# Optimization experiments

Hardware: AMD Instinct MI355X
Metric: run time of the kernel (lower is better)

The kernel has to match this reference:

```python
import jax, jax.numpy as jnp
import numpy as np

N_NODES = 100000
N_EDGES = 1600000
N_GRAPHS = 64
D_IN = 64
D_HID = 64
D_OUT = 64


def gcn_conv(x, W, b, src, dst, n):
    """PyG-style GCNConv: x' = D^-1/2 (A+I) D^-1/2 (x W) + b."""
    xw = x @ W  # [N, d_out]
    loops = jnp.arange(n, dtype=src.dtype)
    s = jnp.concatenate([src, loops])  # add self-loops
    d = jnp.concatenate([dst, loops])
    deg = jax.ops.segment_sum(jnp.ones_like(d, dtype=xw.dtype), d, num_segments=n)
    dinv = jax.lax.rsqrt(jnp.maximum(deg, 1.0))
    coef = dinv[s] * dinv[d]  # [E+N]
    msg = xw[s] * coef[:, None]  # gather + scale, [E+N, d_out]
    out = jax.ops.segment_sum(msg, d, num_segments=n)  # scatter-add
    return out + b


def global_mean_pool(h, batch, num_graphs):
    sums = jax.ops.segment_sum(h, batch, num_segments=num_graphs)
    cnt = jax.ops.segment_sum(jnp.ones((h.shape[0],), h.dtype), batch, num_segments=num_graphs)
    return sums / jnp.maximum(cnt, 1.0)[:, None]


def setup_inputs() -> dict:
    key = jax.random.key(0)
    ks = jax.random.split(key, 8)
    x = jax.random.normal(ks[0], (N_NODES, D_IN), dtype=jnp.float32)
    edge_index = jax.random.randint(ks[1], (2, N_EDGES), 0, N_NODES, dtype=jnp.int64 if jax.config.jax_enable_x64 else jnp.int32)
    batch = jnp.sort(jax.random.randint(ks[2], (N_NODES,), 0, N_GRAPHS))
    sc = lambda fan_in: 1.0 / np.sqrt(fan_in)
    W1 = jax.random.uniform(ks[3], (D_IN, D_HID), jnp.float32, -sc(D_IN), sc(D_IN))
    b1 = jnp.zeros((D_HID,), jnp.float32)
    W2 = jax.random.uniform(ks[4], (D_HID, D_HID), jnp.float32, -sc(D_HID), sc(D_HID))
    b2 = jnp.zeros((D_HID,), jnp.float32)
    Wp = jax.random.uniform(ks[5], (D_HID, D_OUT), jnp.float32, -sc(D_HID), sc(D_HID))
    bp = jax.random.uniform(ks[6], (D_OUT,), jnp.float32, -sc(D_HID), sc(D_HID))
    return {"x": x, "edge_index": edge_index, "batch": batch,
            "W1": W1, "b1": b1, "W2": W2, "b2": b2, "Wp": Wp, "bp": bp}


def reference(x, edge_index, batch, W1, b1, W2, b2, Wp, bp):
    src, dst = edge_index[0], edge_index[1]
    n = x.shape[0]
    h = jax.nn.relu(gcn_conv(x, W1, b1, src, dst, n))
    h = jax.nn.relu(gcn_conv(h, W2, b2, src, dst, n))
    hg = global_mean_pool(h, batch, N_GRAPHS)  # [G, d_hid]
    return hg @ Wp + bp  # [G, d_out]
```

## Files before the change

kernel.cpp:

```cpp
#include <hip/hip_runtime.h>
#include <hip/hip_fp16.h>


#define DF 64
#define BSH 7
#define BNODES 128
#define CAP 4096

struct alignas(8)  h4 { __half2 a, b; };
struct alignas(16) h8 { __half2 a, b, c, d; };


__global__ __launch_bounds__(256) void part_kernel(
        const int* __restrict__ src, const int* __restrict__ dst,
        const int4* __restrict__ src4, const int4* __restrict__ dst4,
        int E, unsigned* __restrict__ bedges, int* __restrict__ bucketCur, int nb) {
    __shared__ int lcnt[1024];
    __shared__ int lbase[1024];
    int tid = threadIdx.x;
    for (int t = tid; t < nb; t += 256) lcnt[t] = 0;
    __syncthreads();
    int nq = E >> 2;
    unsigned packed[32];
    int bkt[32];
    int rk[32];
    int qbase = blockIdx.x * 2048;
#pragma unroll
    for (int c = 0; c < 8; c++) {
        int qi = qbase + c * 256 + tid;
        int4 s = {0, 0, 0, 0}, d = {0, 0, 0, 0};
        bool v = qi < nq;
        if (v) { s = src4[qi]; d = dst4[qi]; }
        packed[4*c+0] = (unsigned)s.x | ((unsigned)(d.x & (BNODES-1)) << 24);
        packed[4*c+1] = (unsigned)s.y | ((unsigned)(d.y & (BNODES-1)) << 24);
        packed[4*c+2] = (unsigned)s.z | ((unsigned)(d.z & (BNODES-1)) << 24);
        packed[4*c+3] = (unsigned)s.w | ((unsigned)(d.w & (BNODES-1)) << 24);
        bkt[4*c+0] = v ? (d.x >> BSH) : -1;
        bkt[4*c+1] = v ? (d.y >> BSH) : -1;
        bkt[4*c+2] = v ? (d.z >> BSH) : -1;
        bkt[4*c+3] = v ? (d.w >> BSH) : -1;
    }
#pragma unroll
    for (int j = 0; j < 32; j++)
        rk[j] = (bkt[j] >= 0) ? atomicAdd(&lcnt[bkt[j]], 1) : 0;
    __syncthreads();
    for (int t = tid; t < nb; t += 256)
        lbase[t] = lcnt[t] ? atomicAdd(&bucketCur[t], lcnt[t]) : 0;
    __syncthreads();
#pragma unroll
    for (int j = 0; j < 32; j++) {
        if (bkt[j] >= 0) {
            int pos = lbase[bkt[j]] + rk[j];
            if (pos < CAP) bedges[(size_t)bkt[j] * CAP + pos] = packed[j];
        }
    }
    if (blockIdx.x == 0 && tid < (E & 3)) {
        int e = nq * 4 + tid;
        int sv = src[e], dv = dst[e];
        int b = dv >> BSH;
        int pos = atomicAdd(&bucketCur[b], 1);
        if (pos < CAP)
            bedges[(size_t)b * CAP + pos] =
                (unsigned)sv | ((unsigned)(dv & (BNODES-1)) << 24);
    }
}

__global__ void part_scalar_kernel(const int* __restrict__ src, const int* __restrict__ dst,
                                   int E, unsigned* __restrict__ bedges,
                                   int* __restrict__ bucketCur) {
    int stride = gridDim.x * blockDim.x;
    for (int e = blockIdx.x * blockDim.x + threadIdx.x; e < E; e += stride) {
        int sv = src[e], dv = dst[e];
        int b = dv >> BSH;
        int pos = atomicAdd(&bucketCur[b], 1);
        if (pos < CAP)
            bedges[(size_t)b * CAP + pos] =
                (unsigned)sv | ((unsigned)(dv & (BNODES-1)) << 24);
    }
}


__global__ __launch_bounds__(256) void sort_kernel(
        unsigned* __restrict__ bedges, const int* __restrict__ bucketCur,
        int* __restrict__ offs, float* __restrict__ dinv, int N) {
    __shared__ unsigned ein[CAP];
    __shared__ unsigned eout[CAP];
    __shared__ int cnt[BNODES];
    __shared__ int sc[BNODES];
    __shared__ int off[BNODES + 1];
    __shared__ int cur[BNODES];
    int b = blockIdx.x, tid = threadIdx.x;
    int n = min(bucketCur[b], CAP);
    unsigned* gp = bedges + (size_t)b * CAP;
    if (tid < BNODES) cnt[tid] = 0;
    __syncthreads();
    for (int i = tid; i < n; i += 256) {
        unsigned u = gp[i];
        ein[i] = u;
        atomicAdd(&cnt[u >> 24], 1);
    }
    __syncthreads();
    if (tid < BNODES) sc[tid] = cnt[tid];
    __syncthreads();
    for (int d = 1; d < BNODES; d <<= 1) {
        int v = (tid >= d && tid < BNODES) ? sc[tid - d] : 0;
        __syncthreads();
        if (tid < BNODES) sc[tid] += v;
        __syncthreads();
    }
    if (tid < BNODES) {
        off[tid + 1] = sc[tid];
        cur[tid] = sc[tid] - cnt[tid];
        if (tid == 0) off[0] = 0;
    }
    __syncthreads();
    for (int i = tid; i < n; i += 256) {
        unsigned u = ein[i];
        int p = atomicAdd(&cur[u >> 24], 1);
        eout[p] = u;
    }
    __syncthreads();
    for (int i = tid; i < n; i += 256) gp[i] = eout[i];
    if (tid <= BNODES) offs[(size_t)b * (BNODES + 1) + tid] = off[tid];
    int node = (b << BSH) + tid;
    if (tid < BNODES && node < N)
        dinv[node] = 1.0f / sqrtf((float)(cnt[tid] + 1));
}


__global__ void gemm_f32in(const float4* __restrict__ X4, const float4* __restrict__ W4,
                           const float* __restrict__ dinv, h4* __restrict__ Y2, int n) {
    __shared__ float4 Wl4[64][16];
    __shared__ float Xl[16][68];
    int tid = threadIdx.x;
    float4* Wf = &Wl4[0][0];
#pragma unroll
    for (int i = 0; i < 4; i++) {
        int idx = tid + i * 256;
        Wf[idx] = W4[idx];
    }
    int row0 = blockIdx.x * 16;
    int r = tid >> 4, c4 = tid & 15;
    {
        int row = row0 + r;
        float4 v = (row < n) ? X4[(size_t)row * 16 + c4] : float4{0.f, 0.f, 0.f, 0.f};
        Xl[r][c4 * 4 + 0] = v.x;
        Xl[r][c4 * 4 + 1] = v.y;
        Xl[r][c4 * 4 + 2] = v.z;
        Xl[r][c4 * 4 + 3] = v.w;
    }
    __syncthreads();
    float ax = 0.f, ay = 0.f, az = 0.f, aw = 0.f;
#pragma unroll
    for (int k = 0; k < 64; k++) {
        float xv = Xl[r][k];
        float4 w = Wl4[k][c4];
        ax += xv * w.x;
        ay += xv * w.y;
        az += xv * w.z;
        aw += xv * w.w;
    }
    int row = row0 + r;
    if (row < n) {
        float dv = dinv[row];
        h4 o;
        o.a = __floats2half2_rn(ax * dv, ay * dv);
        o.b = __floats2half2_rn(az * dv, aw * dv);
        Y2[(size_t)row * 16 + c4] = o;
    }
}

__global__ void gemm_f16in(const h4* __restrict__ X2, const float4* __restrict__ W4,
                           const float* __restrict__ dinv, h4* __restrict__ Y2, int n) {
    __shared__ float4 Wl4[64][16];
    __shared__ float Xl[16][68];
    int tid = threadIdx.x;
    float4* Wf = &Wl4[0][0];
#pragma unroll
    for (int i = 0; i < 4; i++) {
        int idx = tid + i * 256;
        Wf[idx] = W4[idx];
    }
    int row0 = blockIdx.x * 16;
    int r = tid >> 4, c4 = tid & 15;
    {
        int row = row0 + r;
        h4 hv = (row < n) ? X2[(size_t)row * 16 + c4] : h4{__half2{0, 0}, __half2{0, 0}};
        float2 va = __half22float2(hv.a), vb = __half22float2(hv.b);
        Xl[r][c4 * 4 + 0] = va.x;
        Xl[r][c4 * 4 + 1] = va.y;
        Xl[r][c4 * 4 + 2] = vb.x;
        Xl[r][c4 * 4 + 3] = vb.y;
    }
    __syncthreads();
    float ax = 0.f, ay = 0.f, az = 0.f, aw = 0.f;
#pragma unroll
    for (int k = 0; k < 64; k++) {
        float xv = Xl[r][k];
        float4 w = Wl4[k][c4];
        ax += xv * w.x;
        ay += xv * w.y;
        az += xv * w.z;
        aw += xv * w.w;
    }
    int row = row0 + r;
    if (row < n) {
        float dv = dinv[row];
        h4 o;
        o.a = __floats2half2_rn(ax * dv, ay * dv);
        o.b = __floats2half2_rn(az * dv, aw * dv);
        Y2[(size_t)row * 16 + c4] = o;
    }
}

#define ACC8(A, w)                                        \
    { float2 _p = __half22float2((w).a);                  \
      A[0] += _p.x; A[1] += _p.y;                         \
      _p = __half22float2((w).b);                         \
      A[2] += _p.x; A[3] += _p.y;                         \
      _p = __half22float2((w).c);                         \
      A[4] += _p.x; A[5] += _p.y;                         \
      _p = __half22float2((w).d);                         \
      A[6] += _p.x; A[7] += _p.y; }

__global__ __launch_bounds__(256) void agg_kernel(
        const h8* __restrict__ Y8, const unsigned* __restrict__ bedges,
        const int* __restrict__ offs, const float* __restrict__ dinv,
        const float* __restrict__ bias, h8* __restrict__ H8, int N) {
    __shared__ unsigned eb[CAP];
    __shared__ int off[65];
    int blk = blockIdx.x;
    int b = blk >> 1, half = blk & 1;
    int tid = threadIdx.x;
    if (tid < 65) off[tid] = offs[(size_t)b * (BNODES + 1) + half * 64 + tid];
    __syncthreads();
    int e0 = off[0];
    int ecnt = off[64] - e0;
    const unsigned* gp = bedges + (size_t)b * CAP + e0;
    for (int i = tid; i < ecnt; i += 256) eb[i] = gp[i];
    __syncthreads();
    int gg = tid >> 3, q = tid & 7;
    float bq[8];
#pragma unroll
    for (int j = 0; j < 8; j++) bq[j] = bias[q * 8 + j];
#pragma unroll
    for (int rr = 0; rr < 2; rr++) {
        int r = gg + rr * 32;
        int s = off[r] - e0, e = off[r + 1] - e0;
        float A0[8], A1[8], A2[8], A3[8];
#pragma unroll
        for (int j = 0; j < 8; j++) { A0[j] = 0.f; A1[j] = 0.f; A2[j] = 0.f; A3[j] = 0.f; }
        int i = s;
        for (; i + 3 < e; i += 4) {
            unsigned u0 = eb[i], u1 = eb[i + 1], u2 = eb[i + 2], u3 = eb[i + 3];
            h8 w0 = Y8[(size_t)(u0 & 0xFFFFFFu) * 8 + q];
            h8 w1 = Y8[(size_t)(u1 & 0xFFFFFFu) * 8 + q];
            h8 w2 = Y8[(size_t)(u2 & 0xFFFFFFu) * 8 + q];
            h8 w3 = Y8[(size_t)(u3 & 0xFFFFFFu) * 8 + q];
            ACC8(A0, w0); ACC8(A1, w1); ACC8(A2, w2); ACC8(A3, w3);
        }
        for (; i < e; i++) {
            unsigned u = eb[i];
            h8 w = Y8[(size_t)(u & 0xFFFFFFu) * 8 + q];
            ACC8(A0, w);
        }
        int node = (b << BSH) + half * 64 + r;
        if (node < N) {
            h8 sv = Y8[(size_t)node * 8 + q];
            float S[8];
            ACC8(A0, sv);
#pragma unroll
            for (int j = 0; j < 8; j++) S[j] = A0[j] + A1[j] + A2[j] + A3[j];
            float dv = dinv[node];
#pragma unroll
            for (int j = 0; j < 8; j++) S[j] = fmaxf(dv * S[j] + bq[j], 0.f);
            h8 o;
            o.a = __floats2half2_rn(S[0], S[1]);
            o.b = __floats2half2_rn(S[2], S[3]);
            o.c = __floats2half2_rn(S[4], S[5]);
            o.d = __floats2half2_rn(S[6], S[7]);
            H8[(size_t)node * 8 + q] = o;
        }
    }
}


__global__ void pool_kernel(const h4* __restrict__ H2, const int* __restrict__ batch,
                            float* __restrict__ sums, int* __restrict__ cnts, int n) {
    int gw = (blockIdx.x * blockDim.x + threadIdx.x) >> 6;
    int lane = threadIdx.x & 63;
    int g = lane >> 4, q = lane & 15;
    int start = gw * 256;
    if (start >= n) return;
    int end = min(start + 256, n);
    float ax = 0.f, ay = 0.f, az = 0.f, aw = 0.f;
    int cur = -1, run = 0;
    for (int i = start + g; i < end; i += 4) {
        int b = batch[i];
        if (b != cur) {
            if (run > 0) {
                atomicAdd(&sums[cur * DF + q * 4 + 0], ax);
                atomicAdd(&sums[cur * DF + q * 4 + 1], ay);
                atomicAdd(&sums[cur * DF + q * 4 + 2], az);
                atomicAdd(&sums[cur * DF + q * 4 + 3], aw);
                if (q == 0) atomicAdd(&cnts[cur], run);
            }
            cur = b; run = 0;
            ax = ay = az = aw = 0.f;
        }
        h4 hv = H2[(size_t)i * 16 + q];
        float2 va = __half22float2(hv.a), vb = __half22float2(hv.b);
        ax += va.x; ay += va.y; az += vb.x; aw += vb.y;
        run++;
    }
    if (run > 0) {
        atomicAdd(&sums[cur * DF + q * 4 + 0], ax);
        atomicAdd(&sums[cur * DF + q * 4 + 1], ay);
        atomicAdd(&sums[cur * DF + q * 4 + 2], az);
        atomicAdd(&sums[cur * DF + q * 4 + 3], aw);
        if (q == 0) atomicAdd(&cnts[cur], run);
    }
}

__global__ void final_kernel(const float* __restrict__ sums, const int* __restrict__ cnts,
                             const float* __restrict__ Wp, const float* __restrict__ bp,
                             float* __restrict__ out) {
    int g = blockIdx.x, j = threadIdx.x;
    __shared__ float hg[64];
    float c = fmaxf((float)cnts[g], 1.f);
    hg[j] = sums[g * DF + j] / c;
    __syncthreads();
    float acc = bp[j];
#pragma unroll
    for (int k = 0; k < 64; k++) acc += hg[k] * Wp[k * DF + j];
    out[g * DF + j] = acc;
}


extern "C" void kernel_launch(void* const* d_in, const int* in_sizes, int n_in,
                              void* d_out, int out_size, void* d_ws, size_t ws_size,
                              hipStream_t stream) {
    const float* x     = (const float*)d_in[0];
    const int*   ei    = (const int*)d_in[1];
    const int*   batch = (const int*)d_in[2];
    const float* W1    = (const float*)d_in[3];
    const float* b1    = (const float*)d_in[4];
    const float* W2    = (const float*)d_in[5];
    const float* b2    = (const float*)d_in[6];
    const float* Wp    = (const float*)d_in[7];
    const float* bp    = (const float*)d_in[8];

    int N = in_sizes[0] / DF;
    int E = in_sizes[1] / 2;
    const int* src = ei;
    const int* dst = ei + E;
    int NB = (N + BNODES - 1) >> BSH;
    int quadOK = ((E & 3) == 0) && (((uintptr_t)ei & 15) == 0) && (((uintptr_t)dst & 15) == 0);

    char* ws = (char*)d_ws;
    auto alloc = [&](size_t bytes) {
        void* p = (void*)ws;
        ws += (bytes + 255) / 256 * 256;
        return p;
    };
    size_t zBucketCur = 0;
    size_t zPsums     = ((size_t)NB * 4 + 255) / 256 * 256;
    size_t zPcnt      = zPsums + 64 * DF * 4;
    size_t zTotal     = zPcnt + 256;
    char*     zbase     = (char*)alloc(zTotal);
    int*      bucketCur = (int*)(zbase + zBucketCur);
    float*    psums     = (float*)(zbase + zPsums);
    int*      pcnt      = (int*)(zbase + zPcnt);

    float*    dinv      = (float*)alloc((size_t)N * 4);
    unsigned* bedges    = (unsigned*)alloc((size_t)NB * CAP * 4);
    int*      offs      = (int*)alloc((size_t)NB * (BNODES + 1) * 4);
    h4*       y2        = (h4*)alloc((size_t)N * DF * 2);
    h4*       h2        = (h4*)alloc((size_t)N * DF * 2);

    hipMemsetAsync(zbase, 0, zTotal, stream);

    if (quadOK) {
        int nq = E >> 2;
        int pblocks = (nq + 2047) / 2048;
        part_kernel<<<pblocks, 256, 0, stream>>>(src, dst, (const int4*)src, (const int4*)dst,
                                                 E, bedges, bucketCur, NB);
    } else {
        part_scalar_kernel<<<1024, 256, 0, stream>>>(src, dst, E, bedges, bucketCur);
    }
    sort_kernel<<<NB, 256, 0, stream>>>(bedges, bucketCur, offs, dinv, N);

    gemm_f32in<<<(N + 15) / 16, 256, 0, stream>>>((const float4*)x, (const float4*)W1, dinv,
                                                  y2, N);
    agg_kernel<<<2 * NB, 256, 0, stream>>>((const h8*)y2, bedges, offs, dinv,
                                           b1, (h8*)h2, N);
    gemm_f16in<<<(N + 15) / 16, 256, 0, stream>>>(h2, (const float4*)W2, dinv,
                                                  y2, N);
    agg_kernel<<<2 * NB, 256, 0, stream>>>((const h8*)y2, bedges, offs, dinv,
                                           b2, (h8*)h2, N);

    int waves = (N + 255) / 256;
    pool_kernel<<<(waves + 3) / 4, 256, 0, stream>>>(h2, batch, psums, pcnt, N);
    final_kernel<<<64, 64, 0, stream>>>(psums, pcnt, Wp, bp, (float*)d_out);
}
```

Baseline: 242.7 us.

## Split aggregation into quarter-buckets, widen gather unroll, enlarge partition/sort blocks

The aggregation kernel now assigns 32 nodes per block (four blocks per bucket) with one node per 8-thread group. Its gather loop is unrolled to 8 independent loads, and edges beyond a 1024-entry shared stage fall back to global reads. The partition and sort kernels move to 512-thread blocks, and the pooling atomics switch to unsafeAtomicAdd. The aim is more blocks and more memory-level parallelism for the latency-bound gather, with smaller shared memory per block for occupancy, at the cost of more blocks re-reading offsets.

```diff
diff --git a/kernel.cpp b/kernel.cpp
--- a/kernel.cpp
+++ b/kernel.cpp
@@ -6,28 +6,29 @@
 #define BSH 7
 #define BNODES 128
 #define CAP 4096
+#define QCAP 1024
 
 struct alignas(8)  h4 { __half2 a, b; };
 struct alignas(16) h8 { __half2 a, b, c, d; };
 
 
-__global__ __launch_bounds__(256) void part_kernel(
+__global__ __launch_bounds__(512) void part_kernel(
         const int* __restrict__ src, const int* __restrict__ dst,
         const int4* __restrict__ src4, const int4* __restrict__ dst4,
         int E, unsigned* __restrict__ bedges, int* __restrict__ bucketCur, int nb) {
     __shared__ int lcnt[1024];
     __shared__ int lbase[1024];
     int tid = threadIdx.x;
-    for (int t = tid; t < nb; t += 256) lcnt[t] = 0;
+    for (int t = tid; t < nb; t += 512) lcnt[t] = 0;
     __syncthreads();
     int nq = E >> 2;
-    unsigned packed[32];
-    int bkt[32];
-    int rk[32];
+    unsigned packed[16];
+    int bkt[16];
+    int rk[16];
     int qbase = blockIdx.x * 2048;
 #pragma unroll
-    for (int c = 0; c < 8; c++) {
-        int qi = qbase + c * 256 + tid;
+    for (int c = 0; c < 4; c++) {
+        int qi = qbase + c * 512 + tid;
         int4 s = {0, 0, 0, 0}, d = {0, 0, 0, 0};
         bool v = qi < nq;
         if (v) { s = src4[qi]; d = dst4[qi]; }
@@ -41,14 +42,14 @@
         bkt[4*c+3] = v ? (d.w >> BSH) : -1;
     }
 #pragma unroll
-    for (int j = 0; j < 32; j++)
+    for (int j = 0; j < 16; j++)
         rk[j] = (bkt[j] >= 0) ? atomicAdd(&lcnt[bkt[j]], 1) : 0;
     __syncthreads();
-    for (int t = tid; t < nb; t += 256)
+    for (int t = tid; t < nb; t += 512)
         lbase[t] = lcnt[t] ? atomicAdd(&bucketCur[t], lcnt[t]) : 0;
     __syncthreads();
 #pragma unroll
-    for (int j = 0; j < 32; j++) {
+    for (int j = 0; j < 16; j++) {
         if (bkt[j] >= 0) {
             int pos = lbase[bkt[j]] + rk[j];
             if (pos < CAP) bedges[(size_t)bkt[j] * CAP + pos] = packed[j];
@@ -80,7 +81,7 @@
 }
 
 
-__global__ __launch_bounds__(256) void sort_kernel(
+__global__ __launch_bounds__(512) void sort_kernel(
         unsigned* __restrict__ bedges, const int* __restrict__ bucketCur,
         int* __restrict__ offs, float* __restrict__ dinv, int N) {
     __shared__ unsigned ein[CAP];
@@ -94,7 +95,7 @@
     unsigned* gp = bedges + (size_t)b * CAP;
     if (tid < BNODES) cnt[tid] = 0;
     __syncthreads();
-    for (int i = tid; i < n; i += 256) {
+    for (int i = tid; i < n; i += 512) {
         unsigned u = gp[i];
         ein[i] = u;
         atomicAdd(&cnt[u >> 24], 1);
@@ -114,13 +115,13 @@
         if (tid == 0) off[0] = 0;
     }
     __syncthreads();
-    for (int i = tid; i < n; i += 256) {
+    for (int i = tid; i < n; i += 512) {
         unsigned u = ein[i];
         int p = atomicAdd(&cur[u >> 24], 1);
         eout[p] = u;
     }
     __syncthreads();
-    for (int i = tid; i < n; i += 256) gp[i] = eout[i];
+    for (int i = tid; i < n; i += 512) gp[i] = eout[i];
     if (tid <= BNODES) offs[(size_t)b * (BNODES + 1) + tid] = off[tid];
     int node = (b << BSH) + tid;
     if (tid < BNODES && node < N)
@@ -227,61 +228,80 @@
         const h8* __restrict__ Y8, const unsigned* __restrict__ bedges,
         const int* __restrict__ offs, const float* __restrict__ dinv,
         const float* __restrict__ bias, h8* __restrict__ H8, int N) {
-    __shared__ unsigned eb[CAP];
-    __shared__ int off[65];
+    __shared__ unsigned eb[QCAP];
+    __shared__ int off[33];
     int blk = blockIdx.x;
-    int b = blk >> 1, half = blk & 1;
+    int b = blk >> 2, quad = blk & 3;
     int tid = threadIdx.x;
-    if (tid < 65) off[tid] = offs[(size_t)b * (BNODES + 1) + half * 64 + tid];
+    if (tid < 33) off[tid] = offs[(size_t)b * (BNODES + 1) + quad * 32 + tid];
     __syncthreads();
     int e0 = off[0];
-    int ecnt = off[64] - e0;
+    int ecnt = off[32] - e0;
     const unsigned* gp = bedges + (size_t)b * CAP + e0;
-    for (int i = tid; i < ecnt; i += 256) eb[i] = gp[i];
+    int staged = min(ecnt, QCAP);
+    for (int i = tid; i < staged; i += 256) eb[i] = gp[i];
     __syncthreads();
     int gg = tid >> 3, q = tid & 7;
+    int node = (b << BSH) + quad * 32 + gg;
+    if (node >= N) return;
+    int s = off[gg] - e0, e = off[gg + 1] - e0;
+    int e1 = min(e, staged);
     float bq[8];
 #pragma unroll
     for (int j = 0; j < 8; j++) bq[j] = bias[q * 8 + j];
-#pragma unroll
-    for (int rr = 0; rr < 2; rr++) {
-        int r = gg + rr * 32;
-        int s = off[r] - e0, e = off[r + 1] - e0;
-        float A0[8], A1[8], A2[8], A3[8];
-#pragma unroll
-        for (int j = 0; j < 8; j++) { A0[j] = 0.f; A1[j] = 0.f; A2[j] = 0.f; A3[j] = 0.f; }
-        int i = s;
-        for (; i + 3 < e; i += 4) {
-            unsigned u0 = eb[i], u1 = eb[i + 1], u2 = eb[i + 2], u3 = eb[i + 3];
-            h8 w0 = Y8[(size_t)(u0 & 0xFFFFFFu) * 8 + q];
-            h8 w1 = Y8[(size_t)(u1 & 0xFFFFFFu) * 8 + q];
-            h8 w2 = Y8[(size_t)(u2 & 0xFFFFFFu) * 8 + q];
-            h8 w3 = Y8[(size_t)(u3 & 0xFFFFFFu) * 8 + q];
-            ACC8(A0, w0); ACC8(A1, w1); ACC8(A2, w2); ACC8(A3, w3);
-        }
-        for (; i < e; i++) {
-            unsigned u = eb[i];
-            h8 w = Y8[(size_t)(u & 0xFFFFFFu) * 8 + q];
-            ACC8(A0, w);
-        }
-        int node = (b << BSH) + half * 64 + r;
-        if (node < N) {
-            h8 sv = Y8[(size_t)node * 8 + q];
-            float S[8];
-            ACC8(A0, sv);
-#pragma unroll
-            for (int j = 0; j < 8; j++) S[j] = A0[j] + A1[j] + A2[j] + A3[j];
-            float dv = dinv[node];
-#pragma unroll
-            for (int j = 0; j < 8; j++) S[j] = fmaxf(dv * S[j] + bq[j], 0.f);
-            h8 o;
-            o.a = __floats2half2_rn(S[0], S[1]);
-            o.b = __floats2half2_rn(S[2], S[3]);
-            o.c = __floats2half2_rn(S[4], S[5]);
-            o.d = __floats2half2_rn(S[6], S[7]);
-            H8[(size_t)node * 8 + q] = o;
-        }
-    }
+    float A0[8], A1[8], A2[8], A3[8];
+#pragma unroll
+    for (int j = 0; j < 8; j++) { A0[j] = 0.f; A1[j] = 0.f; A2[j] = 0.f; A3[j] = 0.f; }
+    int i = s;
+    for (; i + 7 < e1; i += 8) {
+        unsigned u0 = eb[i],     u1 = eb[i + 1], u2 = eb[i + 2], u3 = eb[i + 3];
+        unsigned u4 = eb[i + 4], u5 = eb[i + 5], u6 = eb[i + 6], u7 = eb[i + 7];
+        h8 w0 = Y8[(size_t)(u0 & 0xFFFFFFu) * 8 + q];
+        h8 w1 = Y8[(size_t)(u1 & 0xFFFFFFu) * 8 + q];
+        h8 w2 = Y8[(size_t)(u2 & 0xFFFFFFu) * 8 + q];
+        h8 w3 = Y8[(size_t)(u3 & 0xFFFFFFu) * 8 + q];
+        h8 w4 = Y8[(size_t)(u4 & 0xFFFFFFu) * 8 + q];
+        h8 w5 = Y8[(size_t)(u5 & 0xFFFFFFu) * 8 + q];
+        h8 w6 = Y8[(size_t)(u6 & 0xFFFFFFu) * 8 + q];
+        h8 w7 = Y8[(size_t)(u7 & 0xFFFFFFu) * 8 + q];
+        ACC8(A0, w0); ACC8(A1, w1); ACC8(A2, w2); ACC8(A3, w3);
+        ACC8(A0, w4); ACC8(A1, w5); ACC8(A2, w6); ACC8(A3, w7);
+    }
+    for (; i + 3 < e1; i += 4) {
+        unsigned u0 = eb[i], u1 = eb[i + 1], u2 = eb[i + 2], u3 = eb[i + 3];
+        h8 w0 = Y8[(size_t)(u0 & 0xFFFFFFu) * 8 + q];
+        h8 w1 = Y8[(size_t)(u1 & 0xFFFFFFu) * 8 + q];
+        h8 w2 = Y8[(size_t)(u2 & 0xFFFFFFu) * 8 + q];
+        h8 w3 = Y8[(size_t)(u3 & 0xFFFFFFu) * 8 + q];
+        ACC8(A0, w0); ACC8(A1, w1); ACC8(A2, w2); ACC8(A3, w3);
+    }
+    for (; i < e1; i++) {
+        unsigned u = eb[i];
+        h8 w = Y8[(size_t)(u & 0xFFFFFFu) * 8 + q];
+        ACC8(A0, w);
+    }
+    for (i = (s > staged ? s : staged); i < e; i++) {
+        unsigned u = gp[i];
+        h8 w = Y8[(size_t)(u & 0xFFFFFFu) * 8 + q];
+        ACC8(A0, w);
+    }
+    h8 sv = Y8[(size_t)node * 8 + q];
+    ACC8(A0, sv);
+    float dv = dinv[node];
+    float t0 = fmaxf(dv * (A0[0] + A1[0] + A2[0] + A3[0]) + bq[0], 0.f);
+    float t1 = fmaxf(dv * (A0[1] + A1[1] + A2[1] + A3[1]) + bq[1], 0.f);
+    float t2 = fmaxf(dv * (A0[2] + A1[2] + A2[2] + A3[2]) + bq[2], 0.f);
+    float t3 = fmaxf(dv * (A0[3] + A1[3] + A2[3] + A3[3]) + bq[3], 0.f);
+    float t4 = fmaxf(dv * (A0[4] + A1[4] + A2[4] + A3[4]) + bq[4], 0.f);
+    float t5 = fmaxf(dv * (A0[5] + A1[5] + A2[5] + A3[5]) + bq[5], 0.f);
+    float t6 = fmaxf(dv * (A0[6] + A1[6] + A2[6] + A3[6]) + bq[6], 0.f);
+    float t7 = fmaxf(dv * (A0[7] + A1[7] + A2[7] + A3[7]) + bq[7], 0.f);
+    h8 o;
+    o.a = __floats2half2_rn(t0, t1);
+    o.b = __floats2half2_rn(t2, t3);
+    o.c = __floats2half2_rn(t4, t5);
+    o.d = __floats2half2_rn(t6, t7);
+    H8[(size_t)node * 8 + q] = o;
 }
 
 
@@ -299,10 +319,10 @@
         int b = batch[i];
         if (b != cur) {
             if (run > 0) {
-                atomicAdd(&sums[cur * DF + q * 4 + 0], ax);
-                atomicAdd(&sums[cur * DF + q * 4 + 1], ay);
-                atomicAdd(&sums[cur * DF + q * 4 + 2], az);
-                atomicAdd(&sums[cur * DF + q * 4 + 3], aw);
+                unsafeAtomicAdd(&sums[cur * DF + q * 4 + 0], ax);
+                unsafeAtomicAdd(&sums[cur * DF + q * 4 + 1], ay);
+                unsafeAtomicAdd(&sums[cur * DF + q * 4 + 2], az);
+                unsafeAtomicAdd(&sums[cur * DF + q * 4 + 3], aw);
                 if (q == 0) atomicAdd(&cnts[cur], run);
             }
             cur = b; run = 0;
@@ -314,10 +334,10 @@
         run++;
     }
     if (run > 0) {
-        atomicAdd(&sums[cur * DF + q * 4 + 0], ax);
-        atomicAdd(&sums[cur * DF + q * 4 + 1], ay);
-        atomicAdd(&sums[cur * DF + q * 4 + 2], az);
-        atomicAdd(&sums[cur * DF + q * 4 + 3], aw);
+        unsafeAtomicAdd(&sums[cur * DF + q * 4 + 0], ax);
+        unsafeAtomicAdd(&sums[cur * DF + q * 4 + 1], ay);
+        unsafeAtomicAdd(&sums[cur * DF + q * 4 + 2], az);
+        unsafeAtomicAdd(&sums[cur * DF + q * 4 + 3], aw);
         if (q == 0) atomicAdd(&cnts[cur], run);
     }
 }
@@ -363,12 +383,11 @@
         ws += (bytes + 255) / 256 * 256;
         return p;
     };
-    size_t zBucketCur = 0;
-    size_t zPsums     = ((size_t)NB * 4 + 255) / 256 * 256;
-    size_t zPcnt      = zPsums + 64 * DF * 4;
-    size_t zTotal     = zPcnt + 256;
+    size_t zPsums = ((size_t)NB * 4 + 255) / 256 * 256;
+    size_t zPcnt  = zPsums + 64 * DF * 4;
+    size_t zTotal = zPcnt + 256;
     char*     zbase     = (char*)alloc(zTotal);
-    int*      bucketCur = (int*)(zbase + zBucketCur);
+    int*      bucketCur = (int*)zbase;
     float*    psums     = (float*)(zbase + zPsums);
     int*      pcnt      = (int*)(zbase + zPcnt);
 
@@ -383,20 +402,20 @@
     if (quadOK) {
         int nq = E >> 2;
         int pblocks = (nq + 2047) / 2048;
-        part_kernel<<<pblocks, 256, 0, stream>>>(src, dst, (const int4*)src, (const int4*)dst,
+        part_kernel<<<pblocks, 512, 0, stream>>>(src, dst, (const int4*)src, (const int4*)dst,
                                                  E, bedges, bucketCur, NB);
     } else {
         part_scalar_kernel<<<1024, 256, 0, stream>>>(src, dst, E, bedges, bucketCur);
     }
-    sort_kernel<<<NB, 256, 0, stream>>>(bedges, bucketCur, offs, dinv, N);
+    sort_kernel<<<NB, 512, 0, stream>>>(bedges, bucketCur, offs, dinv, N);
 
     gemm_f32in<<<(N + 15) / 16, 256, 0, stream>>>((const float4*)x, (const float4*)W1, dinv,
                                                   y2, N);
-    agg_kernel<<<2 * NB, 256, 0, stream>>>((const h8*)y2, bedges, offs, dinv,
+    agg_kernel<<<4 * NB, 256, 0, stream>>>((const h8*)y2, bedges, offs, dinv,
                                            b1, (h8*)h2, N);
     gemm_f16in<<<(N + 15) / 16, 256, 0, stream>>>(h2, (const float4*)W2, dinv,
                                                   y2, N);
-    agg_kernel<<<2 * NB, 256, 0, stream>>>((const h8*)y2, bedges, offs, dinv,
+    agg_kernel<<<4 * NB, 256, 0, stream>>>((const h8*)y2, bedges, offs, dinv,
                                            b2, (h8*)h2, N);
 
     int waves = (N + 255) / 256;
```

Result: slower. 247.9 us (+2.1%).
